# Kernel optimization log

Hardware: AMD Instinct MI355X
Metric: run time of the kernel (lower is better)

Reference implementation:

```python
import jax, jax.numpy as jnp
import numpy as np

N_HEADS = 8

def setup_inputs() -> dict:
    key = jax.random.key(0)
    ks = jax.random.split(key, 7)
    B, S, D = 4, 2048, 512
    s = 1.0 / np.sqrt(D)
    return {
        "input_Q": jax.random.normal(ks[0], (B, S, D), jnp.float32),
        "input_K": jax.random.normal(ks[1], (B, S, D), jnp.float32),
        "input_V": jax.random.normal(ks[2], (B, S, D), jnp.float32),
        "W_Q": jax.random.normal(ks[3], (D, D), jnp.float32) * s,
        "W_K": jax.random.normal(ks[4], (D, D), jnp.float32) * s,
        "W_V": jax.random.normal(ks[5], (D, D), jnp.float32) * s,
        "W_O": jax.random.normal(ks[6], (D, D), jnp.float32) * s,
    }

def reference(input_Q, input_K, input_V, W_Q, W_K, W_V, W_O):
    B, Sq, D = input_Q.shape
    Sk = input_K.shape[1]
    H = N_HEADS
    d_k = D // H
    # torch nn.Linear(bias=False): y = x @ W.T
    def proj(x, W):
        return (x @ W.T).reshape(B, -1, H, d_k).transpose(0, 2, 1, 3)  # [B,H,S,dk]
    Q = proj(input_Q, W_Q)
    K = proj(input_K, W_K)
    V = proj(input_V, W_V)
    scale = 1.0 / jnp.sqrt(jnp.float32(d_k))
    scores = jnp.einsum("bhqd,bhkd->bhqk", Q, K) * scale  # [B,H,Sq,Sk]
    # TriangularCausalMask: mask strict upper triangle with -inf
    causal = jnp.tril(jnp.ones((Sq, Sk), dtype=bool))
    scores = jnp.where(causal[None, None], scores, -jnp.inf)
    attn = jax.nn.softmax(scores, axis=-1)
    context = jnp.einsum("bhqk,bhkd->bhqd", attn, V)
    context = context.transpose(0, 2, 1, 3).reshape(B, Sq, D)
    return context @ W_O.T
```

## Files before the change

kernel.cpp:

```cpp
#include <hip/hip_runtime.h>
#include <hip/hip_bf16.h>
#include <math.h>

#define B_  4
#define S_  2048
#define D_  512
#define H_  8
#define DK_ 64
#define M_  (B_ * S_)

using bf16   = __bf16;
using bf16x4 = __bf16 __attribute__((ext_vector_type(4)));
using bf16x8 = __bf16 __attribute__((ext_vector_type(8)));
using f32x4  = float __attribute__((ext_vector_type(4)));

#define MFMA16(a, b, c) __builtin_amdgcn_mfma_f32_16x16x32_bf16((a), (b), (c), 0, 0, 0)
#define EXP2(x) exp2f(x)

typedef __attribute__((address_space(3))) void       lds_void;
typedef const __attribute__((address_space(1))) void gbl_void;

__device__ __forceinline__ void async16(const bf16* g, bf16* lds) {
    __builtin_amdgcn_global_load_lds((gbl_void*)g, (lds_void*)lds, 16, 0, 0);
}

__device__ __forceinline__ bf16x8 ldg8(const bf16* p) {
    return *reinterpret_cast<const bf16x8*>(p);
}

__device__ __forceinline__ size_t fragbase(int g, int k0, int kk, int t) {
    return ((((size_t)(g * 8 + k0) * 2 + kk) * 4 + t) * 64) * 8;
}

__global__ __launch_bounds__(256) void cvt_all(
    const float* __restrict__ x0, const float* __restrict__ x1, const float* __restrict__ x2,
    const float* __restrict__ w0, const float* __restrict__ w1,
    const float* __restrict__ w2, const float* __restrict__ w3,
    bf16* __restrict__ dst)
{
    const int w    = blockIdx.x * 4 + (threadIdx.x >> 6);
    const int lane = threadIdx.x & 63;
    const int lg = lane >> 4, lc = lane & 15;
    const float* src;
    int c;
    size_t dbase;
    if (w < 24576) {
        const int seg = w >> 13;
        c = w & 8191;
        src = (seg == 0) ? x0 : (seg == 1) ? x1 : x2;
        dbase = (size_t)seg << 22;
    } else {
        const int jj = w - 24576;
        const int seg = jj >> 9;
        c = jj & 511;
        src = (seg == 0) ? w0 : (seg == 1) ? w1 : (seg == 2) ? w2 : w3;
        dbase = ((size_t)3 << 22) + ((size_t)seg << 18);
    }
    const int g = c >> 6, k0 = (c >> 3) & 7, kk = (c >> 2) & 1, t = c & 3;
    const size_t soff = ((size_t)(g * 64 + t * 16 + lc) << 9) + k0 * 64 + kk * 32 + lg * 8;
    f32x4 a = *reinterpret_cast<const f32x4*>(src + soff);
    f32x4 b = *reinterpret_cast<const f32x4*>(src + soff + 4);
    bf16x8 r;
    #pragma unroll
    for (int j = 0; j < 4; ++j) { r[j] = (bf16)a[j]; r[j + 4] = (bf16)b[j]; }
    *reinterpret_cast<bf16x8*>(dst + dbase + ((size_t)c << 9) + (size_t)lane * 8) = r;
}

__global__ __launch_bounds__(256) void gemm_qkv(
    const bf16* __restrict__ Xf, const bf16* __restrict__ Wf,
    bf16* __restrict__ qkv)
{
    const int bx  = blockIdx.x;
    const int xcd = bx & 7;
    const int idx = bx >> 3;
    const int mt  = xcd + 8 * (idx & 7);
    const int rest = idx >> 3;
    const int nt  = rest & 3;
    const int z   = rest >> 2;

    const bf16* Xz = Xf + (size_t)z * M_ * D_;
    const bf16* Wz = Wf + (size_t)z * D_ * D_;
    const bool vz = (z == 2);
    const bf16* A  = vz ? Xz : Wz;
    const bf16* Bm = vz ? Wz : Xz;

    const int lane = threadIdx.x & 63;
    const int wave = threadIdx.x >> 6;
    const int lc = lane & 15;
    const int lg = lane >> 4;
    const int gA = (vz ? 2 * mt : 2 * nt) + (wave >> 1);
    const int gB = (vz ? 2 * nt : 2 * mt) + (wave & 1);

    f32x4 acc[4][4] = {};

    #pragma unroll
    for (int k0 = 0; k0 < 8; ++k0) {
        #pragma unroll
        for (int kk = 0; kk < 2; ++kk) {
            bf16x8 af[4], bfm[4];
            #pragma unroll
            for (int t = 0; t < 4; ++t)
                af[t] = ldg8(A + fragbase(gA, k0, kk, t) + (size_t)lane * 8);
            #pragma unroll
            for (int t = 0; t < 4; ++t)
                bfm[t] = ldg8(Bm + fragbase(gB, k0, kk, t) + (size_t)lane * 8);
            #pragma unroll
            for (int mi = 0; mi < 4; ++mi)
                #pragma unroll
                for (int ni = 0; ni < 4; ++ni)
                    acc[mi][ni] = MFMA16(af[mi], bfm[ni], acc[mi][ni]);
        }
    }

    if (z < 2) {
        bf16* Y = qkv + (size_t)z * M_ * D_;
        const float sc = (z == 0) ? 0.125f * 1.4426950408889634f : 1.0f;
        #pragma unroll
        for (int mi = 0; mi < 4; ++mi)
            #pragma unroll
            for (int ni = 0; ni < 4; ++ni) {
                const int d = gA * 64 + mi * 16 + lg * 4;
                const int s = gB * 64 + ni * 16 + lc;
                bf16x4 v;
                #pragma unroll
                for (int r = 0; r < 4; ++r) v[r] = (bf16)(acc[mi][ni][r] * sc);
                const size_t oidx =
                    ((((size_t)(s >> 11) * H_ + (d >> 6)) * S_
                      + (s & (S_ - 1))) << 6) + (d & 63);
                *reinterpret_cast<bf16x4*>(&Y[oidx]) = v;
            }
    } else {
        bf16* Y = qkv + (size_t)2 * M_ * D_;
        #pragma unroll
        for (int mi = 0; mi < 4; ++mi)
            #pragma unroll
            for (int ni = 0; ni < 4; ++ni) {
                const int s = gA * 64 + mi * 16 + lg * 4;
                const int d = gB * 64 + ni * 16 + lc;
                bf16x4 v;
                #pragma unroll
                for (int r = 0; r < 4; ++r) v[r] = (bf16)acc[mi][ni][r];
                const size_t oidx =
                    ((((size_t)(s >> 11)) * H_ + (d >> 6)) << 17)
                    + (size_t)(d & 63) * S_ + (s & (S_ - 1));
                *reinterpret_cast<bf16x4*>(&Y[oidx]) = v;
            }
    }
}

__global__ __launch_bounds__(256) void gemm_out(
    const bf16* __restrict__ CtxF, const bf16* __restrict__ WoF,
    float* __restrict__ out)
{
    const int bx  = blockIdx.x;
    const int xcd = bx & 7;
    const int idx = bx >> 3;
    const int mt  = xcd + 8 * (idx & 15);
    const int nt  = idx >> 4;

    const int lane = threadIdx.x & 63;
    const int wave = threadIdx.x >> 6;
    const int lc = lane & 15;
    const int lg = lane >> 4;
    const int gA = 2 * nt + (wave >> 1);
    const int tA = (wave & 1) * 2;
    const int gB = mt;

    f32x4 acc[2][4] = {};

    #pragma unroll
    for (int k0 = 0; k0 < 8; ++k0) {
        #pragma unroll
        for (int kk = 0; kk < 2; ++kk) {
            bf16x8 af[2], bfm[4];
            #pragma unroll
            for (int ai = 0; ai < 2; ++ai)
                af[ai] = ldg8(WoF + fragbase(gA, k0, kk, tA + ai) + (size_t)lane * 8);
            #pragma unroll
            for (int t = 0; t < 4; ++t)
                bfm[t] = ldg8(CtxF + fragbase(gB, k0, kk, t) + (size_t)lane * 8);
            #pragma unroll
            for (int ai = 0; ai < 2; ++ai)
                #pragma unroll
                for (int ni = 0; ni < 4; ++ni)
                    acc[ai][ni] = MFMA16(af[ai], bfm[ni], acc[ai][ni]);
        }
    }

    #pragma unroll
    for (int ai = 0; ai < 2; ++ai)
        #pragma unroll
        for (int ni = 0; ni < 4; ++ni) {
            const int d = gA * 64 + (tA + ai) * 16 + lg * 4;
            const int s = gB * 64 + ni * 16 + lc;
            *reinterpret_cast<f32x4*>(&out[(size_t)s * D_ + d]) = acc[ai][ni];
        }
}

__device__ __forceinline__ bf16x8 pfrag(const f32x4 a, const f32x4 b) {
    union U4 { bf16x4 v; unsigned int u[2]; };
    U4 pa, pb;
    #pragma unroll
    for (int r = 0; r < 4; ++r) { pa.v[r] = (bf16)a[r]; pb.v[r] = (bf16)b[r]; }
    auto r0 = __builtin_amdgcn_permlane16_swap(pa.u[0], pb.u[0], false, false);
    auto r1 = __builtin_amdgcn_permlane16_swap(pa.u[1], pb.u[1], false, false);
    union U8 { unsigned int u[4]; bf16x8 v; } out;
    out.u[0] = r0[0]; out.u[1] = r1[0]; out.u[2] = r0[1]; out.u[3] = r1[1];
    return out.v;
}

__global__ __launch_bounds__(512, 4) void attn(
    const bf16* __restrict__ QKV, bf16* __restrict__ CtxF)
{
    const int bx = blockIdx.x;
    const int bh = (bx & 7) * 4 + ((bx >> 3) & 3);
    const int q  = 31 - (bx >> 5);
    const int b = bh >> 3, h = bh & 7;
    const size_t plane = (size_t)S_ * DK_;
    const bf16* Q  = QKV + (size_t)bh * plane;
    const bf16* Kp = QKV + (size_t)(B_ * H_) * plane + (size_t)bh * plane;
    const bf16* Vt = QKV + 2 * (size_t)(B_ * H_) * plane + (size_t)bh * plane;

    const int lane = threadIdx.x & 63;
    const int wave = threadIdx.x >> 6;
    const int wv   = wave & 3;
    const int kh   = wave >> 2;
    const int lc = lane & 15;
    const int lg = lane >> 4;
    const int sg = ((lg & 1) << 1) | (lg >> 1);
    const int mrow = wv * 16 + lc;

    __shared__ bf16 Ks[4][64 * 64];
    __shared__ bf16 Vs[4][64 * 64];

    const int qR = q * 64 + mrow;
    bf16x8 qf0 = ldg8(Q + (size_t)qR * DK_ + lg * 8);
    bf16x8 qf1 = ldg8(Q + (size_t)qR * DK_ + 32 + lg * 8);

    f32x4 accO[4] = {};
    float li = 0.f;

    const int srow = (wave & 3) * 16 + lc;
    const int kc   = (wave >> 2) * 4 + lg;
    const int kcv  = (wave >> 2) * 4 + sg;
    auto stage = [&](int n) {
        const int kn = n * 64;
        async16(Kp + (size_t)(kn + srow) * DK_ + kc * 8,
                Ks[n & 3] + (wave * 64 + lane) * 8);
        async16(Vt + (size_t)srow * S_ + kn + kcv * 8,
                Vs[n & 3] + (wave * 64 + lane) * 8);
    };

    stage(0); stage(1); stage(2);

    for (int j = 0; j <= q; ++j) {
        if (j + 2 <= q)      asm volatile("s_waitcnt vmcnt(4)" ::: "memory");
        else if (j + 1 <= q) asm volatile("s_waitcnt vmcnt(2)" ::: "memory");
        else                 asm volatile("s_waitcnt vmcnt(0)" ::: "memory");
        __builtin_amdgcn_s_barrier();
        if (j + 3 <= q) stage(j + 3);

        const bf16* ks = Ks[j & 3];
        const bf16* vs = Vs[j & 3];

        bf16x8 kf0[2], kf1[2], vf[4];
        #pragma unroll
        for (int tt = 0; tt < 2; ++tt) {
            const int t = 2 * kh + tt;
            kf0[tt] = ldg8(&ks[(t * 64 + lane) * 8]);
            kf1[tt] = ldg8(&ks[(256 + t * 64 + lane) * 8]);
        }
        #pragma unroll
        for (int t = 0; t < 4; ++t)
            vf[t] = ldg8(&vs[(kh * 256 + t * 64 + lane) * 8]);

        f32x4 st[2];
        #pragma unroll
        for (int tt = 0; tt < 2; ++tt) {
            f32x4 zz = {};
            zz = MFMA16(kf0[tt], qf0, zz);
            st[tt] = MFMA16(kf1[tt], qf1, zz);
        }
        float rs = 0.f;
        if (j == q) {
            #pragma unroll
            for (int tt = 0; tt < 2; ++tt)
                #pragma unroll
                for (int r = 0; r < 4; ++r) {
                    const int kl = (2 * kh + tt) * 16 + lg * 4 + r;
                    const float pv = EXP2((kl <= mrow) ? st[tt][r] : -1e30f);
                    st[tt][r] = pv;
                    rs += pv;
                }
        } else {
            #pragma unroll
            for (int tt = 0; tt < 2; ++tt)
                #pragma unroll
                for (int r = 0; r < 4; ++r) {
                    const float pv = EXP2(st[tt][r]);
                    st[tt][r] = pv;
                    rs += pv;
                }
        }
        li += rs;

        const bf16x8 p = pfrag(st[0], st[1]);

        #pragma unroll
        for (int t = 0; t < 4; ++t)
            accO[t] = MFMA16(vf[t], p, accO[t]);
    }

    __syncthreads();
    float* scr = (float*)&Vs[0][0];
    if (kh == 1) {
        float* s = scr + ((size_t)(wv * 64 + lane)) * 17;
        #pragma unroll
        for (int t = 0; t < 4; ++t)
            #pragma unroll
            for (int r = 0; r < 4; ++r) s[t * 4 + r] = accO[t][r];
        s[16] = li;
    }
    __syncthreads();
    if (kh == 0) {
        const float* s = scr + ((size_t)(wv * 64 + lane)) * 17;
        #pragma unroll
        for (int t = 0; t < 4; ++t)
            #pragma unroll
            for (int r = 0; r < 4; ++r) accO[t][r] += s[t * 4 + r];
        li += s[16];
        li += __shfl_xor(li, 16); li += __shfl_xor(li, 32);
        const float rl = 1.0f / li;
        bf16* T = &Ks[0][0] + wv * 1280;

        #pragma unroll
        for (int t = 0; t < 4; ++t) {
            bf16x4 ov;
            #pragma unroll
            for (int r = 0; r < 4; ++r) ov[r] = (bf16)(accO[t][r] * rl);
            *reinterpret_cast<bf16x4*>(&T[lc * 72 + t * 16 + lg * 4]) = ov;
        }
        #pragma unroll
        for (int kk = 0; kk < 2; ++kk) {
            bf16x8 o8 = ldg8(&T[lc * 72 + kk * 32 + lg * 8]);
            *reinterpret_cast<bf16x8*>(
                &CtxF[fragbase(b * 32 + q, h, kk, wv) + (size_t)lane * 8]) = o8;
        }
    }
}

extern "C" void kernel_launch(void* const* d_in, const int* in_sizes, int n_in,
                              void* d_out, int out_size, void* d_ws, size_t ws_size,
                              hipStream_t stream)
{
    float* out = (float*)d_out;

    bf16* Xf   = (bf16*)d_ws;
    bf16* Wf   = Xf + (size_t)3 * M_ * D_;
    bf16* qkv  = Wf + (size_t)4 * D_ * D_;
    bf16* ctxF = qkv + (size_t)3 * M_ * D_;

    cvt_all<<<6656, 256, 0, stream>>>(
        (const float*)d_in[0], (const float*)d_in[1], (const float*)d_in[2],
        (const float*)d_in[3], (const float*)d_in[4], (const float*)d_in[5],
        (const float*)d_in[6], Xf);

    gemm_qkv<<<dim3(768), 256, 0, stream>>>(Xf, Wf, qkv);
    attn<<<dim3(1024), 512, 0, stream>>>(qkv, ctxF);
    gemm_out<<<dim3(512), 256, 0, stream>>>(ctxF, Wf + (size_t)3 * D_ * D_, out);
}
```

Before: 182.8 us.

## Pair causal query tiles per block to share K/V staging and balance work

```diff
diff --git a/kernel.cpp b/kernel.cpp
--- a/kernel.cpp
+++ b/kernel.cpp
@@ -209,12 +209,12 @@
     return out.v;
 }
 
-__global__ __launch_bounds__(512, 4) void attn(
+__global__ __launch_bounds__(1024, 8) void attn(
     const bf16* __restrict__ QKV, bf16* __restrict__ CtxF)
 {
     const int bx = blockIdx.x;
     const int bh = (bx & 7) * 4 + ((bx >> 3) & 3);
-    const int q  = 31 - (bx >> 5);
+    const int pi = bx >> 5;
     const int b = bh >> 3, h = bh & 7;
     const size_t plane = (size_t)S_ * DK_;
     const bf16* Q  = QKV + (size_t)bh * plane;
@@ -223,98 +223,108 @@
 
     const int lane = threadIdx.x & 63;
     const int wave = threadIdx.x >> 6;
-    const int wv   = wave & 3;
-    const int kh   = wave >> 2;
+    const int half = wave >> 3;
+    const int w7   = wave & 7;
+    const int wv   = w7 >> 1;
+    const int kh   = w7 & 1;
     const int lc = lane & 15;
     const int lg = lane >> 4;
     const int sg = ((lg & 1) << 1) | (lg >> 1);
     const int mrow = wv * 16 + lc;
 
-    __shared__ bf16 Ks[4][64 * 64];
-    __shared__ bf16 Vs[4][64 * 64];
-
-    const int qR = q * 64 + mrow;
+    __shared__ bf16 KV[4][2][64 * 64];
+
+    const int lo = pi;
+    const int hi = 31 - pi;
+    const int myq = half ? lo : hi;
+
+    const int qR = myq * 64 + mrow;
     bf16x8 qf0 = ldg8(Q + (size_t)qR * DK_ + lg * 8);
     bf16x8 qf1 = ldg8(Q + (size_t)qR * DK_ + 32 + lg * 8);
 
     f32x4 accO[4] = {};
     float li = 0.f;
 
-    const int srow = (wave & 3) * 16 + lc;
-    const int kc   = (wave >> 2) * 4 + lg;
-    const int kcv  = (wave >> 2) * 4 + sg;
     auto stage = [&](int n) {
         const int kn = n * 64;
-        async16(Kp + (size_t)(kn + srow) * DK_ + kc * 8,
-                Ks[n & 3] + (wave * 64 + lane) * 8);
-        async16(Vt + (size_t)srow * S_ + kn + kcv * 8,
-                Vs[n & 3] + (wave * 64 + lane) * 8);
+        if (half == 0) {
+            const int kc = (w7 >> 2) * 4 + lg;
+            async16(Kp + (size_t)(kn + (w7 & 3) * 16 + lc) * DK_ + kc * 8,
+                    &KV[n & 3][0][(w7 * 64 + lane) * 8]);
+        } else {
+            const int kcv = (w7 >> 2) * 4 + sg;
+            async16(Vt + (size_t)((w7 & 3) * 16 + lc) * S_ + kn + kcv * 8,
+                    &KV[n & 3][1][(w7 * 64 + lane) * 8]);
+        }
     };
 
     stage(0); stage(1); stage(2);
 
-    for (int j = 0; j <= q; ++j) {
-        if (j + 2 <= q)      asm volatile("s_waitcnt vmcnt(4)" ::: "memory");
-        else if (j + 1 <= q) asm volatile("s_waitcnt vmcnt(2)" ::: "memory");
-        else                 asm volatile("s_waitcnt vmcnt(0)" ::: "memory");
+    for (int j = 0; j <= hi; ++j) {
+        if (j + 2 <= hi)      asm volatile("s_waitcnt vmcnt(2)" ::: "memory");
+        else if (j + 1 <= hi) asm volatile("s_waitcnt vmcnt(1)" ::: "memory");
+        else                  asm volatile("s_waitcnt vmcnt(0)" ::: "memory");
         __builtin_amdgcn_s_barrier();
-        if (j + 3 <= q) stage(j + 3);
-
-        const bf16* ks = Ks[j & 3];
-        const bf16* vs = Vs[j & 3];
-
-        bf16x8 kf0[2], kf1[2], vf[4];
-        #pragma unroll
-        for (int tt = 0; tt < 2; ++tt) {
-            const int t = 2 * kh + tt;
-            kf0[tt] = ldg8(&ks[(t * 64 + lane) * 8]);
-            kf1[tt] = ldg8(&ks[(256 + t * 64 + lane) * 8]);
-        }
-        #pragma unroll
-        for (int t = 0; t < 4; ++t)
-            vf[t] = ldg8(&vs[(kh * 256 + t * 64 + lane) * 8]);
-
-        f32x4 st[2];
-        #pragma unroll
-        for (int tt = 0; tt < 2; ++tt) {
-            f32x4 zz = {};
-            zz = MFMA16(kf0[tt], qf0, zz);
-            st[tt] = MFMA16(kf1[tt], qf1, zz);
-        }
-        float rs = 0.f;
-        if (j == q) {
-            #pragma unroll
-            for (int tt = 0; tt < 2; ++tt)
-                #pragma unroll
-                for (int r = 0; r < 4; ++r) {
-                    const int kl = (2 * kh + tt) * 16 + lg * 4 + r;
-                    const float pv = EXP2((kl <= mrow) ? st[tt][r] : -1e30f);
-                    st[tt][r] = pv;
-                    rs += pv;
-                }
-        } else {
-            #pragma unroll
-            for (int tt = 0; tt < 2; ++tt)
-                #pragma unroll
-                for (int r = 0; r < 4; ++r) {
-                    const float pv = EXP2(st[tt][r]);
-                    st[tt][r] = pv;
-                    rs += pv;
-                }
-        }
-        li += rs;
-
-        const bf16x8 p = pfrag(st[0], st[1]);
-
-        #pragma unroll
-        for (int t = 0; t < 4; ++t)
-            accO[t] = MFMA16(vf[t], p, accO[t]);
+        if (j + 3 <= hi) stage(j + 3);
+
+        if (j <= myq) {
+            const bf16* ks = KV[j & 3][0];
+            const bf16* vs = KV[j & 3][1];
+
+            bf16x8 kf0[2], kf1[2], vf[4];
+            #pragma unroll
+            for (int tt = 0; tt < 2; ++tt) {
+                const int t = 2 * kh + tt;
+                kf0[tt] = ldg8(&ks[(t * 64 + lane) * 8]);
+                kf1[tt] = ldg8(&ks[(256 + t * 64 + lane) * 8]);
+            }
+            #pragma unroll
+            for (int t = 0; t < 4; ++t)
+                vf[t] = ldg8(&vs[(kh * 256 + t * 64 + lane) * 8]);
+
+            f32x4 st[2];
+            #pragma unroll
+            for (int tt = 0; tt < 2; ++tt) {
+                f32x4 zz = {};
+                zz = MFMA16(kf0[tt], qf0, zz);
+                st[tt] = MFMA16(kf1[tt], qf1, zz);
+            }
+            float rs = 0.f;
+            if (j == myq) {
+                #pragma unroll
+                for (int tt = 0; tt < 2; ++tt)
+                    #pragma unroll
+                    for (int r = 0; r < 4; ++r) {
+                        const int kl = (2 * kh + tt) * 16 + lg * 4 + r;
+                        const float pv = EXP2((kl <= mrow) ? st[tt][r] : -1e30f);
+                        st[tt][r] = pv;
+                        rs += pv;
+                    }
+            } else {
+                #pragma unroll
+                for (int tt = 0; tt < 2; ++tt)
+                    #pragma unroll
+                    for (int r = 0; r < 4; ++r) {
+                        const float pv = EXP2(st[tt][r]);
+                        st[tt][r] = pv;
+                        rs += pv;
+                    }
+            }
+            li += rs;
+
+            const bf16x8 p = pfrag(st[0], st[1]);
+
+            #pragma unroll
+            for (int t = 0; t < 4; ++t)
+                accO[t] = MFMA16(vf[t], p, accO[t]);
+        }
     }
 
     __syncthreads();
-    float* scr = (float*)&Vs[0][0];
+    float* scr = (float*)&KV[0][0][0];
+    const int slot = (half * 4 + wv) * 64 + lane;
     if (kh == 1) {
-        float* s = scr + ((size_t)(wv * 64 + lane)) * 17;
+        float* s = scr + (size_t)slot * 17;
         #pragma unroll
         for (int t = 0; t < 4; ++t)
             #pragma unroll
@@ -323,7 +333,7 @@
     }
     __syncthreads();
     if (kh == 0) {
-        const float* s = scr + ((size_t)(wv * 64 + lane)) * 17;
+        const float* s = scr + (size_t)slot * 17;
         #pragma unroll
         for (int t = 0; t < 4; ++t)
             #pragma unroll
@@ -331,7 +341,7 @@
         li += s[16];
         li += __shfl_xor(li, 16); li += __shfl_xor(li, 32);
         const float rl = 1.0f / li;
-        bf16* T = &Ks[0][0] + wv * 1280;
+        bf16* T = (bf16*)((char*)&KV[0][0][0] + 36864) + (half * 4 + wv) * 1280;
 
         #pragma unroll
         for (int t = 0; t < 4; ++t) {
@@ -344,7 +354,7 @@
         for (int kk = 0; kk < 2; ++kk) {
             bf16x8 o8 = ldg8(&T[lc * 72 + kk * 32 + lg * 8]);
             *reinterpret_cast<bf16x8*>(
-                &CtxF[fragbase(b * 32 + q, h, kk, wv) + (size_t)lane * 8]) = o8;
+                &CtxF[fragbase(b * 32 + myq, h, kk, wv) + (size_t)lane * 8]) = o8;
         }
     }
 }
@@ -366,6 +376,6 @@
         (const float*)d_in[6], Xf);
 
     gemm_qkv<<<dim3(768), 256, 0, stream>>>(Xf, Wf, qkv);
-    attn<<<dim3(1024), 512, 0, stream>>>(qkv, ctxF);
+    attn<<<dim3(512), 1024, 0, stream>>>(qkv, ctxF);
     gemm_out<<<dim3(512), 256, 0, stream>>>(ctxF, Wf + (size_t)3 * D_ * D_, out);
 }
```

After: 190.6 us. +4.3%, slower.
